# Performance work log

Hardware: AMD Instinct MI355X
Metric: run time of the kernel (lower is better)

The kernel has to match this reference:

```python
import jax, jax.numpy as jnp
import numpy as np

B, V = 256, 128000


def setup_inputs() -> dict:
    key = jax.random.key(0)
    k1, k2 = jax.random.split(key)
    logits = jax.random.normal(k1, (B, V), dtype=jnp.float32) * 4.0
    # temperatures in [0.3, 1.2] to avoid division by ~0
    temperatures = jax.random.uniform(k2, (B,), dtype=jnp.float32) * 0.9 + 0.3
    return {"logits": logits, "temperatures": temperatures}


def reference(logits, temperatures):
    # temperature-scaled softmax
    x = logits.astype(jnp.float32) / temperatures[:, None]
    probs = jax.nn.softmax(x, axis=-1)  # (B, V)
    # torch.empty_like(probs).exponential_(1).clamp_min_(1e-10)
    noise = jnp.maximum(
        jax.random.exponential(jax.random.key(42), probs.shape, dtype=jnp.float32),
        1e-10,
    )
    # Gumbel-max style sampling: argmax of probs / Exp(1) noise
    return jnp.argmax(probs / noise, axis=-1)  # (B,) int
```

## Files before the change

kernel.cpp:

```cpp
#include <hip/hip_runtime.h>
#include <stdint.h>
#include <math.h>

#define BB 256
#define ROW 128000
#define SPLIT 4
#define CHUNK (ROW / SPLIT)
#define THREADS 512
#define WAVES (THREADS / 64)
#define GRID (BB * SPLIT)

__device__ __forceinline__ uint32_t rotl32(uint32_t x, int r) {
    return (x << r) | (x >> (32 - r));
}

#define TF_K2 0x1BD11BF0u

__device__ __forceinline__ void threefry4_xor(uint32_t c, uint32_t bits[4]) {
    uint32_t x0[4], x1[4];
#pragma unroll
    for (int j = 0; j < 4; ++j) {
        x0[j] = 0u;
        x1[j] = c + (uint32_t)j + 42u;
    }

#define ROUND4(r)                                     \
    do {                                              \
        _Pragma("unroll")                             \
        for (int j = 0; j < 4; ++j) {                 \
            x0[j] += x1[j];                           \
            x1[j] = rotl32(x1[j], (r));               \
            x1[j] ^= x0[j];                           \
        }                                             \
    } while (0)
#define INJ4(a, b)                                    \
    do {                                              \
        _Pragma("unroll")                             \
        for (int j = 0; j < 4; ++j) {                 \
            x0[j] += (a);                             \
            x1[j] += (b);                             \
        }                                             \
    } while (0)

    ROUND4(13); ROUND4(15); ROUND4(26); ROUND4(6);
    INJ4(42u, TF_K2 + 1u);
    ROUND4(17); ROUND4(29); ROUND4(16); ROUND4(24);
    INJ4(TF_K2, 2u);
    ROUND4(13); ROUND4(15); ROUND4(26); ROUND4(6);
    INJ4(0u, 45u);
    ROUND4(17); ROUND4(29); ROUND4(16); ROUND4(24);
    INJ4(42u, TF_K2 + 4u);
    ROUND4(13); ROUND4(15); ROUND4(26); ROUND4(6);
    INJ4(TF_K2, 5u);

#undef ROUND4
#undef INJ4

#pragma unroll
    for (int j = 0; j < 4; ++j) bits[j] = x0[j] ^ x1[j];
}

__device__ __forceinline__ uint32_t f2o(float f) {
    uint32_t u = __float_as_uint(f);
    return (u & 0x80000000u) ? ~u : (u | 0x80000000u);
}

__device__ __forceinline__ float log_exp_noise(uint32_t bits) {
    const float uf = __uint_as_float(0x3F800000u | (bits >> 9));
    const float u = uf - 1.0f;
    const float m = 2.0f - uf;
    const float lg_m = __builtin_amdgcn_logf(m);
    const float es =
        u * fmaf(u, fmaf(u, fmaf(u, fmaf(u, 0.2f, 0.25f), 0.33333333333f), 0.5f), 1.0f);
    const bool small = (u < 0.0625f);
    float P = small ? es : -lg_m;
    const float csel = small ? 0.0f : -0.36651292058166432701f;
    P = fmaxf(P, 1e-10f);
    return fmaf(0.69314718055994530942f, __builtin_amdgcn_logf(P), csel);
}

__global__ __launch_bounds__(THREADS, 8) void sampler_kernel(
    const float* __restrict__ logits,
    const float* __restrict__ temps,
    unsigned long long* __restrict__ ws) {
    const int g = blockIdx.x;
    const int b = g >> 2;
    const int q = g & 3;
    const float invT = 1.0f / temps[b];
    const float* rowp = logits + (size_t)b * ROW + (size_t)q * CHUNK;
    const uint32_t cbase = (uint32_t)b * (uint32_t)ROW + (uint32_t)q * CHUNK;

    float best_s = -INFINITY;
    uint32_t best_v = 0u;
    const int tid = threadIdx.x;

#pragma unroll 1
    for (int t = 0; t < (CHUNK + THREADS * 4 - 1) / (THREADS * 4); ++t) {
        const int vl = t * THREADS * 4 + tid * 4;
        if (vl < CHUNK) {
            const float4 x4 = *reinterpret_cast<const float4*>(rowp + vl);
            const float xs[4] = {x4.x, x4.y, x4.z, x4.w};

            uint32_t bits[4];
            threefry4_xor(cbase + (uint32_t)vl, bits);

            float s[4];
#pragma unroll
            for (int j = 0; j < 4; ++j)
                s[j] = fmaf(xs[j], invT, -log_exp_noise(bits[j]));

#pragma unroll
            for (int j = 0; j < 4; ++j) {
                const uint32_t v = (uint32_t)(q * CHUNK + vl) + (uint32_t)j;
                if (s[j] > best_s) { best_s = s[j]; best_v = v; }
            }
        }
    }

    unsigned long long best =
        ((unsigned long long)f2o(best_s) << 32) | (uint32_t)(~best_v);

#pragma unroll
    for (int off = 32; off >= 1; off >>= 1) {
        const unsigned long long o = __shfl_xor(best, off);
        best = (o > best) ? o : best;
    }

    __shared__ unsigned long long sbest[WAVES];
    const int lane = tid & 63;
    const int wid = tid >> 6;
    if (lane == 0) sbest[wid] = best;
    __syncthreads();

    if (tid == 0) {
        unsigned long long r = sbest[0];
#pragma unroll
        for (int w = 1; w < WAVES; ++w) r = (sbest[w] > r) ? sbest[w] : r;
        ws[g] = r;
    }
}

__global__ __launch_bounds__(BB) void combine_kernel(
    const unsigned long long* __restrict__ ws, int* __restrict__ out) {
    const int b = threadIdx.x;
    const unsigned long long* p = ws + b * SPLIT;
    unsigned long long r = p[0];
#pragma unroll
    for (int w = 1; w < SPLIT; ++w) r = (p[w] > r) ? p[w] : r;
    out[b] = (int)(~(uint32_t)(r & 0xFFFFFFFFull));
}

extern "C" void kernel_launch(void* const* d_in, const int* in_sizes, int n_in,
                              void* d_out, int out_size, void* d_ws, size_t ws_size,
                              hipStream_t stream) {
    const float* logits = (const float*)d_in[0];
    const float* temps = (const float*)d_in[1];
    int* out = (int*)d_out;
    unsigned long long* ws = (unsigned long long*)d_ws;

    hipLaunchKernelGGL(sampler_kernel, dim3(GRID), dim3(THREADS), 0, stream,
                       logits, temps, ws);
    hipLaunchKernelGGL(combine_kernel, dim3(1), dim3(BB), 0, stream, ws, out);
}
```

Measured before the change: 93.52 us.

## Restructure threefry to 8-wide with folded injections and exact-fit tiling

Changes the split to 5 blocks per row with 640 threads that each handle 8 elements over exactly 5 iterations, which removes the bounds check. The threefry rounds are algebraically folded: the zero first round is simplified, key injections are merged into the following round, rotations use alignbit, and the final injection is applied at output. The noise log computation is simplified by switching the log2 scaling and shortening the series with a smaller threshold. These cut ALU work in a compute-bound RNG kernel, at the cost of higher register pressure from the 8-wide state and the removed occupancy hint.

Result: slower. 117.6 us (+25.8%).

```diff
diff --git a/kernel.cpp b/kernel.cpp
--- a/kernel.cpp
+++ b/kernel.cpp
@@ -4,60 +4,63 @@
 
 #define BB 256
 #define ROW 128000
-#define SPLIT 4
+#define SPLIT 5
 #define CHUNK (ROW / SPLIT)
-#define THREADS 512
+#define THREADS 640
 #define WAVES (THREADS / 64)
+#define ITERS 5
 #define GRID (BB * SPLIT)
-
-__device__ __forceinline__ uint32_t rotl32(uint32_t x, int r) {
-    return (x << r) | (x >> (32 - r));
-}
 
 #define TF_K2 0x1BD11BF0u
 
-__device__ __forceinline__ void threefry4_xor(uint32_t c, uint32_t bits[4]) {
-    uint32_t x0[4], x1[4];
+__device__ __forceinline__ uint32_t rotl32(uint32_t x, int r) {
+    return __builtin_amdgcn_alignbit(x, x, 32 - r);
+}
+
+__device__ __forceinline__ void threefry8_xor(uint32_t c, uint32_t bits[8]) {
+    uint32_t x0[8], x1[8];
 #pragma unroll
-    for (int j = 0; j < 4; ++j) {
-        x0[j] = 0u;
-        x1[j] = c + (uint32_t)j + 42u;
+    for (int j = 0; j < 8; ++j) x1[j] = c + (uint32_t)j + 42u;
+
+#pragma unroll
+    for (int j = 0; j < 8; ++j) {
+        x0[j] = x1[j];
+        x1[j] = rotl32(x1[j], 13) ^ x0[j];
     }
 
-#define ROUND4(r)                                     \
+#define RND(r)                                        \
     do {                                              \
         _Pragma("unroll")                             \
-        for (int j = 0; j < 4; ++j) {                 \
+        for (int j = 0; j < 8; ++j) {                 \
             x0[j] += x1[j];                           \
-            x1[j] = rotl32(x1[j], (r));               \
-            x1[j] ^= x0[j];                           \
+            x1[j] = rotl32(x1[j], (r)) ^ x0[j];       \
         }                                             \
     } while (0)
-#define INJ4(a, b)                                    \
+#define RNDI(r, A, B)                                 \
     do {                                              \
         _Pragma("unroll")                             \
-        for (int j = 0; j < 4; ++j) {                 \
-            x0[j] += (a);                             \
-            x1[j] += (b);                             \
+        for (int j = 0; j < 8; ++j) {                 \
+            x1[j] += (B);                             \
+            x0[j] = x0[j] + (A) + x1[j];              \
+            x1[j] = rotl32(x1[j], (r)) ^ x0[j];       \
         }                                             \
     } while (0)
 
-    ROUND4(13); ROUND4(15); ROUND4(26); ROUND4(6);
-    INJ4(42u, TF_K2 + 1u);
-    ROUND4(17); ROUND4(29); ROUND4(16); ROUND4(24);
-    INJ4(TF_K2, 2u);
-    ROUND4(13); ROUND4(15); ROUND4(26); ROUND4(6);
-    INJ4(0u, 45u);
-    ROUND4(17); ROUND4(29); ROUND4(16); ROUND4(24);
-    INJ4(42u, TF_K2 + 4u);
-    ROUND4(13); ROUND4(15); ROUND4(26); ROUND4(6);
-    INJ4(TF_K2, 5u);
+    RND(15); RND(26); RND(6);
+    RNDI(17, 42u, TF_K2 + 1u);
+    RND(29); RND(16); RND(24);
+    RNDI(13, TF_K2, 2u);
+    RND(15); RND(26); RND(6);
+    RNDI(17, 0u, 45u);
+    RND(29); RND(16); RND(24);
+    RNDI(13, 42u, TF_K2 + 4u);
+    RND(15); RND(26); RND(6);
 
-#undef ROUND4
-#undef INJ4
+#undef RND
+#undef RNDI
 
 #pragma unroll
-    for (int j = 0; j < 4; ++j) bits[j] = x0[j] ^ x1[j];
+    for (int j = 0; j < 8; ++j) bits[j] = (x0[j] + TF_K2) ^ (x1[j] + 5u);
 }
 
 __device__ __forceinline__ uint32_t f2o(float f) {
@@ -65,27 +68,26 @@
     return (u & 0x80000000u) ? ~u : (u | 0x80000000u);
 }
 
-__device__ __forceinline__ float log_exp_noise(uint32_t bits) {
+__device__ __forceinline__ float neg_log_exp_noise(uint32_t bits) {
     const float uf = __uint_as_float(0x3F800000u | (bits >> 9));
     const float u = uf - 1.0f;
     const float m = 2.0f - uf;
     const float lg_m = __builtin_amdgcn_logf(m);
-    const float es =
-        u * fmaf(u, fmaf(u, fmaf(u, fmaf(u, 0.2f, 0.25f), 0.33333333333f), 0.5f), 1.0f);
-    const bool small = (u < 0.0625f);
-    float P = small ? es : -lg_m;
-    const float csel = small ? 0.0f : -0.36651292058166432701f;
-    P = fmaxf(P, 1e-10f);
-    return fmaf(0.69314718055994530942f, __builtin_amdgcn_logf(P), csel);
+    const float E_main = -0.69314718055994530942f * lg_m;
+    const float E_ser =
+        u * fmaf(u, fmaf(u, fmaf(u, 0.25f, 0.33333333333f), 0.5f), 1.0f);
+    float E = (u < 0.03125f) ? E_ser : E_main;
+    E = fmaxf(E, 1e-10f);
+    return -0.69314718055994530942f * __builtin_amdgcn_logf(E);
 }
 
-__global__ __launch_bounds__(THREADS, 8) void sampler_kernel(
+__global__ __launch_bounds__(THREADS) void sampler_kernel(
     const float* __restrict__ logits,
     const float* __restrict__ temps,
     unsigned long long* __restrict__ ws) {
     const int g = blockIdx.x;
-    const int b = g >> 2;
-    const int q = g & 3;
+    const int b = g / SPLIT;
+    const int q = g - b * SPLIT;
     const float invT = 1.0f / temps[b];
     const float* rowp = logits + (size_t)b * ROW + (size_t)q * CHUNK;
     const uint32_t cbase = (uint32_t)b * (uint32_t)ROW + (uint32_t)q * CHUNK;
@@ -95,25 +97,24 @@
     const int tid = threadIdx.x;
 
 #pragma unroll 1
-    for (int t = 0; t < (CHUNK + THREADS * 4 - 1) / (THREADS * 4); ++t) {
-        const int vl = t * THREADS * 4 + tid * 4;
-        if (vl < CHUNK) {
-            const float4 x4 = *reinterpret_cast<const float4*>(rowp + vl);
-            const float xs[4] = {x4.x, x4.y, x4.z, x4.w};
+    for (int t = 0; t < ITERS; ++t) {
+        const int vl = t * THREADS * 8 + tid * 8;
+        const float4 xa = *reinterpret_cast<const float4*>(rowp + vl);
+        const float4 xb = *reinterpret_cast<const float4*>(rowp + vl + 4);
+        const float xs[8] = {xa.x, xa.y, xa.z, xa.w, xb.x, xb.y, xb.z, xb.w};
 
-            uint32_t bits[4];
-            threefry4_xor(cbase + (uint32_t)vl, bits);
+        uint32_t bits[8];
+        threefry8_xor(cbase + (uint32_t)vl, bits);
 
-            float s[4];
+        float s[8];
 #pragma unroll
-            for (int j = 0; j < 4; ++j)
-                s[j] = fmaf(xs[j], invT, -log_exp_noise(bits[j]));
+        for (int j = 0; j < 8; ++j)
+            s[j] = fmaf(xs[j], invT, neg_log_exp_noise(bits[j]));
 
+        const uint32_t vb = (uint32_t)(q * CHUNK + vl);
 #pragma unroll
-            for (int j = 0; j < 4; ++j) {
-                const uint32_t v = (uint32_t)(q * CHUNK + vl) + (uint32_t)j;
-                if (s[j] > best_s) { best_s = s[j]; best_v = v; }
-            }
+        for (int j = 0; j < 8; ++j) {
+            if (s[j] > best_s) { best_s = s[j]; best_v = vb | (uint32_t)j; }
         }
     }
 
```
